# Optimization experiments

Hardware: AMD Instinct MI355X
Metric: run time of the kernel (lower is better)

Reference implementation:

```python
import jax, jax.numpy as jnp
import numpy as np

MARGIN = 0.2

def _pdist(a, b):
    # euclidean distance matrix, matches pdist_torch (clamp at 1e-12 then sqrt)
    d2 = (a * a).sum(1)[:, None] + (b * b).sum(1)[None, :] - 2.0 * (a @ b.T)
    return jnp.sqrt(jnp.clip(d2, 1e-12))

def setup_inputs() -> dict:
    key = jax.random.key(0)
    P, K, D = 128, 16, 4096  # identities, samples-per-identity, feature dim
    inputs = jax.random.normal(key, (4 * P * K, D), dtype=jnp.float32)
    # labels laid out [modality, identity, sample] so torch.chunk grouping is valid
    targets = jnp.tile(jnp.repeat(jnp.arange(P, dtype=jnp.int64), K), 4)
    return {"inputs": inputs, "targets": targets, "num_classes": P}

def reference(inputs, targets, num_classes):
    P = int(num_classes)
    total, D = inputs.shape
    K = total // (4 * P)
    # per-modality, per-identity centers: [4, P, D]
    c = inputs.reshape(4, P, K, D).mean(axis=2)
    c1, c2, c3, c4 = c[0], c[1], c[2], c[3]

    eye = jnp.eye(P, dtype=bool)
    offdiag_min = lambda d: jnp.min(jnp.where(eye, jnp.inf, d), axis=1)
    # unique labels => mask is identity => masked max/min over mask[i] is the diagonal
    ap123 = jnp.diagonal(_pdist(c2, c3))
    an123 = jax.lax.stop_gradient(jnp.diagonal(_pdist(c1, c3)))  # .detach()
    an33 = offdiag_min(_pdist(c3, c3))
    an11 = offdiag_min(_pdist(c1, c1))
    ap124 = jnp.diagonal(_pdist(c1, c4))
    an124 = jax.lax.stop_gradient(jnp.diagonal(_pdist(c2, c4)))  # .detach()
    an44 = offdiag_min(_pdist(c4, c4))
    an22 = offdiag_min(_pdist(c2, c2))

    # MarginRankingLoss(margin)(x1=an, x2=ap, y=1) = mean(relu(ap - an + margin))
    mrl = lambda an, ap: jnp.mean(jnp.maximum(ap - an + MARGIN, 0.0))
    loss_123 = mrl(an123, ap123) + 0.5 * (mrl(an33, ap123) + mrl(an11, ap123))
    loss_124 = mrl(an124, ap124) + 0.5 * (mrl(an44, ap124) + mrl(an22, ap124))
    return (loss_123 + loss_124) / 2
```

## Files before the change

kernel.cpp:

```cpp
#include <hip/hip_runtime.h>
#include <math.h>

#define P_IDS 128
#define D_DIM 4096
#define MARGIN_F 0.2f
#define NCHUNK 32

__global__ __launch_bounds__(128) void centers_kernel(const float* __restrict__ in,
                                                      float* __restrict__ c, int K) {
    const int b  = blockIdx.x;
    const int ds = blockIdx.y;
    const float* src = in + (size_t)b * K * D_DIM + ds * 512;
    float* dst = c + (size_t)b * D_DIM + ds * 512;
    const float inv = 1.0f / (float)K;
    float4 acc = make_float4(0.f, 0.f, 0.f, 0.f);
    const int t = threadIdx.x;
    for (int k = 0; k < K; ++k) {
        float4 v = reinterpret_cast<const float4*>(src + (size_t)k * D_DIM)[t];
        acc.x += v.x; acc.y += v.y; acc.z += v.z; acc.w += v.w;
    }
    acc.x *= inv; acc.y *= inv; acc.z *= inv; acc.w *= inv;
    reinterpret_cast<float4*>(dst)[t] = acc;
}

__global__ __launch_bounds__(256) void pair_partial_kernel(const float* __restrict__ c,
                                                           float* __restrict__ part) {
    __shared__ float As[64][68];
    __shared__ float Bs[64][68];
    const int tid = threadIdx.x;
    const int tx = tid & 15, ty = tid >> 4;
    const int bx = blockIdx.x;
    const int m = bx >> 2, it = (bx >> 1) & 1, jt = bx & 1;
    const int dc = blockIdx.y;
    const float* cm = c + (size_t)m * P_IDS * D_DIM;
    const float* gA = cm + (size_t)(it * 64) * D_DIM;
    const float* gB = cm + (size_t)(jt * 64) * D_DIM;

    float acc[4][4];
    #pragma unroll
    for (int r = 0; r < 4; ++r)
        #pragma unroll
        for (int s = 0; s < 4; ++s) acc[r][s] = 0.f;

    for (int ch = 0; ch < 2; ++ch) {
        const int dbase = dc * 128 + ch * 64;
        __syncthreads();
        #pragma unroll
        for (int idx = 0; idx < 4; ++idx) {
            int li = idx * 256 + tid;
            int row = li >> 4, c4 = li & 15;
            float4 va = *reinterpret_cast<const float4*>(gA + (size_t)row * D_DIM + dbase + c4 * 4);
            float4 vb = *reinterpret_cast<const float4*>(gB + (size_t)row * D_DIM + dbase + c4 * 4);
            *reinterpret_cast<float4*>(&As[row][c4 * 4]) = va;
            *reinterpret_cast<float4*>(&Bs[row][c4 * 4]) = vb;
        }
        __syncthreads();
        #pragma unroll
        for (int d4 = 0; d4 < 16; ++d4) {
            float4 a[4], b[4];
            #pragma unroll
            for (int r = 0; r < 4; ++r)
                a[r] = *reinterpret_cast<const float4*>(&As[ty * 4 + r][d4 * 4]);
            #pragma unroll
            for (int s = 0; s < 4; ++s)
                b[s] = *reinterpret_cast<const float4*>(&Bs[s * 16 + tx][d4 * 4]);
            #pragma unroll
            for (int r = 0; r < 4; ++r)
                #pragma unroll
                for (int s = 0; s < 4; ++s) {
                    float dx = a[r].x - b[s].x, dy = a[r].y - b[s].y;
                    float dz = a[r].z - b[s].z, dw = a[r].w - b[s].w;
                    acc[r][s] = fmaf(dx, dx, acc[r][s]);
                    acc[r][s] = fmaf(dy, dy, acc[r][s]);
                    acc[r][s] = fmaf(dz, dz, acc[r][s]);
                    acc[r][s] = fmaf(dw, dw, acc[r][s]);
                }
        }
    }
    float* pbase = part + ((size_t)dc * 4 + m) * P_IDS * P_IDS;
    #pragma unroll
    for (int r = 0; r < 4; ++r) {
        int i = it * 64 + ty * 4 + r;
        #pragma unroll
        for (int s = 0; s < 4; ++s) {
            int j = jt * 64 + s * 16 + tx;
            pbase[i * P_IDS + j] = acc[r][s];
        }
    }
}

__global__ __launch_bounds__(256) void rowmin_kernel(const float* __restrict__ part,
                                                     float* __restrict__ anmin) {
    const int tid = threadIdx.x;
    const int rowid = blockIdx.x * 2 + (tid >> 7);
    const int j = tid & 127;
    const size_t base = (size_t)rowid * P_IDS + j;
    float sum = 0.f;
    #pragma unroll 4
    for (int dc = 0; dc < NCHUNK; ++dc)
        sum += part[(size_t)dc * 4 * P_IDS * P_IDS + base];
    float d = sqrtf(fmaxf(sum, 1e-12f));
    if (j == (rowid & (P_IDS - 1))) d = INFINITY;
    #pragma unroll
    for (int off = 32; off > 0; off >>= 1) d = fminf(d, __shfl_down(d, off, 64));
    __shared__ float wmin[4];
    if ((tid & 63) == 0) wmin[tid >> 6] = d;
    __syncthreads();
    if (tid == 0) {
        anmin[blockIdx.x * 2]     = fminf(wmin[0], wmin[1]);
        anmin[blockIdx.x * 2 + 1] = fminf(wmin[2], wmin[3]);
    }
}

__global__ __launch_bounds__(256) void diag_kernel(const float* __restrict__ c,
                                                   float* __restrict__ diag) {
    const int i = blockIdx.x;
    const size_t PD = (size_t)P_IDS * D_DIM;
    const float4* r1 = reinterpret_cast<const float4*>(c + 0 * PD + (size_t)i * D_DIM);
    const float4* r2 = reinterpret_cast<const float4*>(c + 1 * PD + (size_t)i * D_DIM);
    const float4* r3 = reinterpret_cast<const float4*>(c + 2 * PD + (size_t)i * D_DIM);
    const float4* r4 = reinterpret_cast<const float4*>(c + 3 * PD + (size_t)i * D_DIM);
    float a23 = 0.f, a13 = 0.f, a14 = 0.f, a24 = 0.f;
    for (int t = threadIdx.x; t < (D_DIM >> 2); t += 256) {
        float4 v1 = r1[t], v2 = r2[t], v3 = r3[t], v4 = r4[t];
        float dx, dy, dz, dw;
        dx = v2.x - v3.x; dy = v2.y - v3.y; dz = v2.z - v3.z; dw = v2.w - v3.w;
        a23 = fmaf(dx, dx, a23); a23 = fmaf(dy, dy, a23);
        a23 = fmaf(dz, dz, a23); a23 = fmaf(dw, dw, a23);
        dx = v1.x - v3.x; dy = v1.y - v3.y; dz = v1.z - v3.z; dw = v1.w - v3.w;
        a13 = fmaf(dx, dx, a13); a13 = fmaf(dy, dy, a13);
        a13 = fmaf(dz, dz, a13); a13 = fmaf(dw, dw, a13);
        dx = v1.x - v4.x; dy = v1.y - v4.y; dz = v1.z - v4.z; dw = v1.w - v4.w;
        a14 = fmaf(dx, dx, a14); a14 = fmaf(dy, dy, a14);
        a14 = fmaf(dz, dz, a14); a14 = fmaf(dw, dw, a14);
        dx = v2.x - v4.x; dy = v2.y - v4.y; dz = v2.z - v4.z; dw = v2.w - v4.w;
        a24 = fmaf(dx, dx, a24); a24 = fmaf(dy, dy, a24);
        a24 = fmaf(dz, dz, a24); a24 = fmaf(dw, dw, a24);
    }
    const int wave = threadIdx.x >> 6, lane = threadIdx.x & 63;
    #pragma unroll
    for (int off = 32; off > 0; off >>= 1) {
        a23 += __shfl_down(a23, off, 64);
        a13 += __shfl_down(a13, off, 64);
        a14 += __shfl_down(a14, off, 64);
        a24 += __shfl_down(a24, off, 64);
    }
    __shared__ float red[4][4];
    if (lane == 0) { red[wave][0] = a23; red[wave][1] = a13; red[wave][2] = a14; red[wave][3] = a24; }
    __syncthreads();
    if (threadIdx.x == 0) {
        float s23 = red[0][0] + red[1][0] + red[2][0] + red[3][0];
        float s13 = red[0][1] + red[1][1] + red[2][1] + red[3][1];
        float s14 = red[0][2] + red[1][2] + red[2][2] + red[3][2];
        float s24 = red[0][3] + red[1][3] + red[2][3] + red[3][3];
        diag[0 * P_IDS + i] = sqrtf(fmaxf(s23, 1e-12f));
        diag[1 * P_IDS + i] = sqrtf(fmaxf(s13, 1e-12f));
        diag[2 * P_IDS + i] = sqrtf(fmaxf(s14, 1e-12f));
        diag[3 * P_IDS + i] = sqrtf(fmaxf(s24, 1e-12f));
    }
}

__global__ __launch_bounds__(128) void loss_kernel(const float* __restrict__ anmin,
                                                   const float* __restrict__ diag,
                                                   float* __restrict__ out) {
    const int i = threadIdx.x;
    float ap123 = diag[0 * P_IDS + i], an123 = diag[1 * P_IDS + i];
    float ap124 = diag[2 * P_IDS + i], an124 = diag[3 * P_IDS + i];
    float an11 = anmin[0 * P_IDS + i], an22 = anmin[1 * P_IDS + i];
    float an33 = anmin[2 * P_IDS + i], an44 = anmin[3 * P_IDS + i];
    float s = fmaxf(ap123 - an123 + MARGIN_F, 0.f)
            + 0.5f * (fmaxf(ap123 - an33 + MARGIN_F, 0.f) +
                      fmaxf(ap123 - an11 + MARGIN_F, 0.f))
            + fmaxf(ap124 - an124 + MARGIN_F, 0.f)
            + 0.5f * (fmaxf(ap124 - an44 + MARGIN_F, 0.f) +
                      fmaxf(ap124 - an22 + MARGIN_F, 0.f));
    #pragma unroll
    for (int off = 32; off > 0; off >>= 1) s += __shfl_down(s, off, 64);
    __shared__ float w[2];
    if ((threadIdx.x & 63) == 0) w[threadIdx.x >> 6] = s;
    __syncthreads();
    if (threadIdx.x == 0) out[0] = (w[0] + w[1]) / (2.0f * (float)P_IDS);
}

extern "C" void kernel_launch(void* const* d_in, const int* in_sizes, int n_in,
                              void* d_out, int out_size, void* d_ws, size_t ws_size,
                              hipStream_t stream) {
    const float* in = (const float*)d_in[0];
    const int N = in_sizes[1];
    const int K = N / (4 * P_IDS);

    float* c     = (float*)d_ws;
    float* part  = c + (size_t)4 * P_IDS * D_DIM;
    float* anmin = part + (size_t)NCHUNK * 4 * P_IDS * P_IDS;
    float* diag  = anmin + 4 * P_IDS;

    hipLaunchKernelGGL(centers_kernel, dim3(4 * P_IDS, 8), dim3(128), 0, stream, in, c, K);
    hipLaunchKernelGGL(pair_partial_kernel, dim3(16, NCHUNK), dim3(256), 0, stream, c, part);
    hipLaunchKernelGGL(rowmin_kernel, dim3(2 * P_IDS), dim3(256), 0, stream, part, anmin);
    hipLaunchKernelGGL(diag_kernel, dim3(P_IDS), dim3(256), 0, stream, c, diag);
    hipLaunchKernelGGL(loss_kernel, dim3(1), dim3(128), 0, stream, anmin, diag, (float*)d_out);
}
```

Measured before the change: 52.50 us.

## Fuse all stages into one cooperative persistent kernel with grid syncs

Replaces the five separate kernel launches with a single cooperative kernel of 256 blocks × 512 threads that runs centers, pairwise partial distances, row-min and diagonal reductions, and the final loss, separated by grid.sync(). The number of reduction chunks drops from 32 to 16 to fit the 256-block grid, which halves the partial-buffer traffic, and the diagonal distances are split one pair per wave. The aim is to remove per-launch overhead and inter-kernel gaps. In exchange it pays grid-wide barrier costs, uses fewer, larger blocks in the pair phase, and falls back to four ordinary launches if the cooperative launch fails.

```diff
diff --git a/kernel.cpp b/kernel.cpp
--- a/kernel.cpp
+++ b/kernel.cpp
@@ -1,71 +1,82 @@
 #include <hip/hip_runtime.h>
+#include <hip/hip_cooperative_groups.h>
 #include <math.h>
+
+namespace cg = cooperative_groups;
 
 #define P_IDS 128
 #define D_DIM 4096
+#define K_SMP 16
 #define MARGIN_F 0.2f
-#define NCHUNK 32
-
-__global__ __launch_bounds__(128) void centers_kernel(const float* __restrict__ in,
-                                                      float* __restrict__ c, int K) {
-    const int b  = blockIdx.x;
-    const int ds = blockIdx.y;
-    const float* src = in + (size_t)b * K * D_DIM + ds * 512;
-    float* dst = c + (size_t)b * D_DIM + ds * 512;
-    const float inv = 1.0f / (float)K;
-    float4 acc = make_float4(0.f, 0.f, 0.f, 0.f);
-    const int t = threadIdx.x;
-    for (int k = 0; k < K; ++k) {
-        float4 v = reinterpret_cast<const float4*>(src + (size_t)k * D_DIM)[t];
-        acc.x += v.x; acc.y += v.y; acc.z += v.z; acc.w += v.w;
-    }
-    acc.x *= inv; acc.y *= inv; acc.z *= inv; acc.w *= inv;
-    reinterpret_cast<float4*>(dst)[t] = acc;
-}
-
-__global__ __launch_bounds__(256) void pair_partial_kernel(const float* __restrict__ c,
-                                                           float* __restrict__ part) {
-    __shared__ float As[64][68];
-    __shared__ float Bs[64][68];
-    const int tid = threadIdx.x;
+#define NCHUNK 16
+
+__device__ __forceinline__ void dev_centers(const float* __restrict__ in,
+                                            float* __restrict__ c,
+                                            int blk, int tid) {
+    const float inv = 1.0f / (float)K_SMP;
+    #pragma unroll
+    for (int r = 0; r < 2; ++r) {
+        const int row = blk * 2 + r;
+        const float* src = in + (size_t)row * K_SMP * D_DIM;
+        float* dst = c + (size_t)row * D_DIM;
+        float4 acc0 = make_float4(0.f, 0.f, 0.f, 0.f);
+        float4 acc1 = make_float4(0.f, 0.f, 0.f, 0.f);
+        #pragma unroll 4
+        for (int k = 0; k < K_SMP; ++k) {
+            const float4* s4 = reinterpret_cast<const float4*>(src + (size_t)k * D_DIM);
+            float4 v0 = s4[tid], v1 = s4[512 + tid];
+            acc0.x += v0.x; acc0.y += v0.y; acc0.z += v0.z; acc0.w += v0.w;
+            acc1.x += v1.x; acc1.y += v1.y; acc1.z += v1.z; acc1.w += v1.w;
+        }
+        acc0.x *= inv; acc0.y *= inv; acc0.z *= inv; acc0.w *= inv;
+        acc1.x *= inv; acc1.y *= inv; acc1.z *= inv; acc1.w *= inv;
+        reinterpret_cast<float4*>(dst)[tid]       = acc0;
+        reinterpret_cast<float4*>(dst)[512 + tid] = acc1;
+    }
+}
+
+__device__ __forceinline__ void dev_pair(const float* __restrict__ c,
+                                         float* __restrict__ part,
+                                         int blk, int tid,
+                                         float (*As)[68], float (*Bs)[68]) {
+    const int bx = blk & 15;
+    const int dc = blk >> 4;
+    const int m = bx >> 2, it = (bx >> 1) & 1, jt = bx & 1;
     const int tx = tid & 15, ty = tid >> 4;
-    const int bx = blockIdx.x;
-    const int m = bx >> 2, it = (bx >> 1) & 1, jt = bx & 1;
-    const int dc = blockIdx.y;
     const float* cm = c + (size_t)m * P_IDS * D_DIM;
     const float* gA = cm + (size_t)(it * 64) * D_DIM;
     const float* gB = cm + (size_t)(jt * 64) * D_DIM;
 
-    float acc[4][4];
-    #pragma unroll
-    for (int r = 0; r < 4; ++r)
+    float acc[2][4];
+    #pragma unroll
+    for (int r = 0; r < 2; ++r)
         #pragma unroll
         for (int s = 0; s < 4; ++s) acc[r][s] = 0.f;
 
-    for (int ch = 0; ch < 2; ++ch) {
-        const int dbase = dc * 128 + ch * 64;
+    for (int ch = 0; ch < 4; ++ch) {
+        const int dbase = dc * 256 + ch * 64;
         __syncthreads();
         #pragma unroll
-        for (int idx = 0; idx < 4; ++idx) {
-            int li = idx * 256 + tid;
+        for (int idx = 0; idx < 2; ++idx) {
+            int li = idx * 512 + tid;
             int row = li >> 4, c4 = li & 15;
-            float4 va = *reinterpret_cast<const float4*>(gA + (size_t)row * D_DIM + dbase + c4 * 4);
-            float4 vb = *reinterpret_cast<const float4*>(gB + (size_t)row * D_DIM + dbase + c4 * 4);
-            *reinterpret_cast<float4*>(&As[row][c4 * 4]) = va;
-            *reinterpret_cast<float4*>(&Bs[row][c4 * 4]) = vb;
+            *reinterpret_cast<float4*>(&As[row][c4 * 4]) =
+                *reinterpret_cast<const float4*>(gA + (size_t)row * D_DIM + dbase + c4 * 4);
+            *reinterpret_cast<float4*>(&Bs[row][c4 * 4]) =
+                *reinterpret_cast<const float4*>(gB + (size_t)row * D_DIM + dbase + c4 * 4);
         }
         __syncthreads();
         #pragma unroll
         for (int d4 = 0; d4 < 16; ++d4) {
-            float4 a[4], b[4];
+            float4 a[2], b[4];
             #pragma unroll
-            for (int r = 0; r < 4; ++r)
-                a[r] = *reinterpret_cast<const float4*>(&As[ty * 4 + r][d4 * 4]);
+            for (int r = 0; r < 2; ++r)
+                a[r] = *reinterpret_cast<const float4*>(&As[ty * 2 + r][d4 * 4]);
             #pragma unroll
             for (int s = 0; s < 4; ++s)
                 b[s] = *reinterpret_cast<const float4*>(&Bs[s * 16 + tx][d4 * 4]);
             #pragma unroll
-            for (int r = 0; r < 4; ++r)
+            for (int r = 0; r < 2; ++r)
                 #pragma unroll
                 for (int s = 0; s < 4; ++s) {
                     float dx = a[r].x - b[s].x, dy = a[r].y - b[s].y;
@@ -77,10 +88,10 @@
                 }
         }
     }
-    float* pbase = part + ((size_t)dc * 4 + m) * P_IDS * P_IDS;
-    #pragma unroll
-    for (int r = 0; r < 4; ++r) {
-        int i = it * 64 + ty * 4 + r;
+    float* pbase = part + ((size_t)dc * 4 + m) * (P_IDS * P_IDS);
+    #pragma unroll
+    for (int r = 0; r < 2; ++r) {
+        int i = it * 64 + ty * 2 + r;
         #pragma unroll
         for (int s = 0; s < 4; ++s) {
             int j = jt * 64 + s * 16 + tx;
@@ -89,114 +100,150 @@
     }
 }
 
-__global__ __launch_bounds__(256) void rowmin_kernel(const float* __restrict__ part,
-                                                     float* __restrict__ anmin) {
-    const int tid = threadIdx.x;
-    const int rowid = blockIdx.x * 2 + (tid >> 7);
-    const int j = tid & 127;
-    const size_t base = (size_t)rowid * P_IDS + j;
-    float sum = 0.f;
-    #pragma unroll 4
-    for (int dc = 0; dc < NCHUNK; ++dc)
-        sum += part[(size_t)dc * 4 * P_IDS * P_IDS + base];
-    float d = sqrtf(fmaxf(sum, 1e-12f));
-    if (j == (rowid & (P_IDS - 1))) d = INFINITY;
+__device__ __forceinline__ void dev_rowmin(const float* __restrict__ part,
+                                           float* __restrict__ anmin,
+                                           int blk, int tid) {
+    __shared__ float wmin[8];
+    float d = INFINITY;
+    if (tid < 256) {
+        const int rowid = blk * 2 + (tid >> 7);
+        const int j = tid & 127;
+        const size_t base = (size_t)(rowid >> 7) * (P_IDS * P_IDS) +
+                            (size_t)(rowid & 127) * P_IDS + j;
+        float sum = 0.f;
+        #pragma unroll 4
+        for (int dc = 0; dc < NCHUNK; ++dc)
+            sum += part[(size_t)dc * 4 * P_IDS * P_IDS + base];
+        d = sqrtf(fmaxf(sum, 1e-12f));
+        if (j == (rowid & (P_IDS - 1))) d = INFINITY;
+    }
     #pragma unroll
     for (int off = 32; off > 0; off >>= 1) d = fminf(d, __shfl_down(d, off, 64));
-    __shared__ float wmin[4];
     if ((tid & 63) == 0) wmin[tid >> 6] = d;
     __syncthreads();
     if (tid == 0) {
-        anmin[blockIdx.x * 2]     = fminf(wmin[0], wmin[1]);
-        anmin[blockIdx.x * 2 + 1] = fminf(wmin[2], wmin[3]);
-    }
-}
-
-__global__ __launch_bounds__(256) void diag_kernel(const float* __restrict__ c,
-                                                   float* __restrict__ diag) {
-    const int i = blockIdx.x;
+        anmin[blk * 2]     = fminf(wmin[0], wmin[1]);
+        anmin[blk * 2 + 1] = fminf(wmin[2], wmin[3]);
+    }
+}
+
+__device__ __forceinline__ void dev_diag(const float* __restrict__ c,
+                                         float* __restrict__ diag,
+                                         int i, int tid) {
+    const int wave = tid >> 6, lane = tid & 63;
+    if (wave >= 4) return;
+    const int am = (wave == 0 || wave == 3) ? 1 : 0;
+    const int bm = (wave <= 1) ? 2 : 3;
     const size_t PD = (size_t)P_IDS * D_DIM;
-    const float4* r1 = reinterpret_cast<const float4*>(c + 0 * PD + (size_t)i * D_DIM);
-    const float4* r2 = reinterpret_cast<const float4*>(c + 1 * PD + (size_t)i * D_DIM);
-    const float4* r3 = reinterpret_cast<const float4*>(c + 2 * PD + (size_t)i * D_DIM);
-    const float4* r4 = reinterpret_cast<const float4*>(c + 3 * PD + (size_t)i * D_DIM);
-    float a23 = 0.f, a13 = 0.f, a14 = 0.f, a24 = 0.f;
-    for (int t = threadIdx.x; t < (D_DIM >> 2); t += 256) {
-        float4 v1 = r1[t], v2 = r2[t], v3 = r3[t], v4 = r4[t];
-        float dx, dy, dz, dw;
-        dx = v2.x - v3.x; dy = v2.y - v3.y; dz = v2.z - v3.z; dw = v2.w - v3.w;
-        a23 = fmaf(dx, dx, a23); a23 = fmaf(dy, dy, a23);
-        a23 = fmaf(dz, dz, a23); a23 = fmaf(dw, dw, a23);
-        dx = v1.x - v3.x; dy = v1.y - v3.y; dz = v1.z - v3.z; dw = v1.w - v3.w;
-        a13 = fmaf(dx, dx, a13); a13 = fmaf(dy, dy, a13);
-        a13 = fmaf(dz, dz, a13); a13 = fmaf(dw, dw, a13);
-        dx = v1.x - v4.x; dy = v1.y - v4.y; dz = v1.z - v4.z; dw = v1.w - v4.w;
-        a14 = fmaf(dx, dx, a14); a14 = fmaf(dy, dy, a14);
-        a14 = fmaf(dz, dz, a14); a14 = fmaf(dw, dw, a14);
-        dx = v2.x - v4.x; dy = v2.y - v4.y; dz = v2.z - v4.z; dw = v2.w - v4.w;
-        a24 = fmaf(dx, dx, a24); a24 = fmaf(dy, dy, a24);
-        a24 = fmaf(dz, dz, a24); a24 = fmaf(dw, dw, a24);
-    }
-    const int wave = threadIdx.x >> 6, lane = threadIdx.x & 63;
-    #pragma unroll
-    for (int off = 32; off > 0; off >>= 1) {
-        a23 += __shfl_down(a23, off, 64);
-        a13 += __shfl_down(a13, off, 64);
-        a14 += __shfl_down(a14, off, 64);
-        a24 += __shfl_down(a24, off, 64);
-    }
-    __shared__ float red[4][4];
-    if (lane == 0) { red[wave][0] = a23; red[wave][1] = a13; red[wave][2] = a14; red[wave][3] = a24; }
+    const float4* ra = reinterpret_cast<const float4*>(c + am * PD + (size_t)i * D_DIM);
+    const float4* rb = reinterpret_cast<const float4*>(c + bm * PD + (size_t)i * D_DIM);
+    float acc = 0.f;
+    #pragma unroll
+    for (int t = 0; t < 16; ++t) {
+        float4 a = ra[t * 64 + lane];
+        float4 b = rb[t * 64 + lane];
+        float dx = a.x - b.x, dy = a.y - b.y, dz = a.z - b.z, dw = a.w - b.w;
+        acc = fmaf(dx, dx, acc); acc = fmaf(dy, dy, acc);
+        acc = fmaf(dz, dz, acc); acc = fmaf(dw, dw, acc);
+    }
+    #pragma unroll
+    for (int off = 32; off > 0; off >>= 1) acc += __shfl_down(acc, off, 64);
+    if (lane == 0) diag[wave * P_IDS + i] = sqrtf(fmaxf(acc, 1e-12f));
+}
+
+__device__ __forceinline__ void dev_loss(const float* __restrict__ anmin,
+                                         const float* __restrict__ diag,
+                                         float* __restrict__ out, int tid) {
+    __shared__ float w[8];
+    float s = 0.f;
+    if (tid < 128) {
+        const int i = tid;
+        float ap123 = diag[0 * P_IDS + i], an123 = diag[1 * P_IDS + i];
+        float ap124 = diag[2 * P_IDS + i], an124 = diag[3 * P_IDS + i];
+        float an11 = anmin[0 * P_IDS + i], an22 = anmin[1 * P_IDS + i];
+        float an33 = anmin[2 * P_IDS + i], an44 = anmin[3 * P_IDS + i];
+        s = fmaxf(ap123 - an123 + MARGIN_F, 0.f)
+          + 0.5f * (fmaxf(ap123 - an33 + MARGIN_F, 0.f) +
+                    fmaxf(ap123 - an11 + MARGIN_F, 0.f))
+          + fmaxf(ap124 - an124 + MARGIN_F, 0.f)
+          + 0.5f * (fmaxf(ap124 - an44 + MARGIN_F, 0.f) +
+                    fmaxf(ap124 - an22 + MARGIN_F, 0.f));
+    }
+    #pragma unroll
+    for (int off = 32; off > 0; off >>= 1) s += __shfl_down(s, off, 64);
+    if ((tid & 63) == 0) w[tid >> 6] = s;
     __syncthreads();
-    if (threadIdx.x == 0) {
-        float s23 = red[0][0] + red[1][0] + red[2][0] + red[3][0];
-        float s13 = red[0][1] + red[1][1] + red[2][1] + red[3][1];
-        float s14 = red[0][2] + red[1][2] + red[2][2] + red[3][2];
-        float s24 = red[0][3] + red[1][3] + red[2][3] + red[3][3];
-        diag[0 * P_IDS + i] = sqrtf(fmaxf(s23, 1e-12f));
-        diag[1 * P_IDS + i] = sqrtf(fmaxf(s13, 1e-12f));
-        diag[2 * P_IDS + i] = sqrtf(fmaxf(s14, 1e-12f));
-        diag[3 * P_IDS + i] = sqrtf(fmaxf(s24, 1e-12f));
-    }
-}
-
-__global__ __launch_bounds__(128) void loss_kernel(const float* __restrict__ anmin,
-                                                   const float* __restrict__ diag,
-                                                   float* __restrict__ out) {
-    const int i = threadIdx.x;
-    float ap123 = diag[0 * P_IDS + i], an123 = diag[1 * P_IDS + i];
-    float ap124 = diag[2 * P_IDS + i], an124 = diag[3 * P_IDS + i];
-    float an11 = anmin[0 * P_IDS + i], an22 = anmin[1 * P_IDS + i];
-    float an33 = anmin[2 * P_IDS + i], an44 = anmin[3 * P_IDS + i];
-    float s = fmaxf(ap123 - an123 + MARGIN_F, 0.f)
-            + 0.5f * (fmaxf(ap123 - an33 + MARGIN_F, 0.f) +
-                      fmaxf(ap123 - an11 + MARGIN_F, 0.f))
-            + fmaxf(ap124 - an124 + MARGIN_F, 0.f)
-            + 0.5f * (fmaxf(ap124 - an44 + MARGIN_F, 0.f) +
-                      fmaxf(ap124 - an22 + MARGIN_F, 0.f));
-    #pragma unroll
-    for (int off = 32; off > 0; off >>= 1) s += __shfl_down(s, off, 64);
-    __shared__ float w[2];
-    if ((threadIdx.x & 63) == 0) w[threadIdx.x >> 6] = s;
-    __syncthreads();
-    if (threadIdx.x == 0) out[0] = (w[0] + w[1]) / (2.0f * (float)P_IDS);
+    if (tid == 0)
+        out[0] = (w[0] + w[1] + w[2] + w[3] + w[4] + w[5] + w[6] + w[7])
+               / (2.0f * (float)P_IDS);
+}
+
+__global__ __launch_bounds__(512) void cpm_fused(const float* __restrict__ in,
+                                                 float* __restrict__ c,
+                                                 float* __restrict__ part,
+                                                 float* __restrict__ anmin,
+                                                 float* __restrict__ diag,
+                                                 float* __restrict__ out) {
+    cg::grid_group grid = cg::this_grid();
+    __shared__ float As[64][68];
+    __shared__ float Bs[64][68];
+    const int tid = threadIdx.x;
+    const int blk = blockIdx.x;
+
+    dev_centers(in, c, blk, tid);
+    grid.sync();
+    dev_pair(c, part, blk, tid, As, Bs);
+    grid.sync();
+    dev_rowmin(part, anmin, blk, tid);
+    if (blk < 128) dev_diag(c, diag, blk, tid);
+    grid.sync();
+    if (blk == 0) dev_loss(anmin, diag, out, tid);
+}
+
+__global__ __launch_bounds__(512) void k_centers(const float* __restrict__ in,
+                                                 float* __restrict__ c) {
+    dev_centers(in, c, blockIdx.x, threadIdx.x);
+}
+__global__ __launch_bounds__(512) void k_pair(const float* __restrict__ c,
+                                              float* __restrict__ part) {
+    __shared__ float As[64][68];
+    __shared__ float Bs[64][68];
+    dev_pair(c, part, blockIdx.x, threadIdx.x, As, Bs);
+}
+__global__ __launch_bounds__(512) void k_red(const float* __restrict__ part,
+                                             const float* __restrict__ c,
+                                             float* __restrict__ anmin,
+                                             float* __restrict__ diag) {
+    dev_rowmin(part, anmin, blockIdx.x, threadIdx.x);
+    if (blockIdx.x < 128) dev_diag(c, diag, blockIdx.x, threadIdx.x);
+}
+__global__ __launch_bounds__(512) void k_loss(const float* __restrict__ anmin,
+                                              const float* __restrict__ diag,
+                                              float* __restrict__ out) {
+    dev_loss(anmin, diag, out, threadIdx.x);
 }
 
 extern "C" void kernel_launch(void* const* d_in, const int* in_sizes, int n_in,
                               void* d_out, int out_size, void* d_ws, size_t ws_size,
                               hipStream_t stream) {
     const float* in = (const float*)d_in[0];
-    const int N = in_sizes[1];
-    const int K = N / (4 * P_IDS);
 
     float* c     = (float*)d_ws;
     float* part  = c + (size_t)4 * P_IDS * D_DIM;
     float* anmin = part + (size_t)NCHUNK * 4 * P_IDS * P_IDS;
     float* diag  = anmin + 4 * P_IDS;
-
-    hipLaunchKernelGGL(centers_kernel, dim3(4 * P_IDS, 8), dim3(128), 0, stream, in, c, K);
-    hipLaunchKernelGGL(pair_partial_kernel, dim3(16, NCHUNK), dim3(256), 0, stream, c, part);
-    hipLaunchKernelGGL(rowmin_kernel, dim3(2 * P_IDS), dim3(256), 0, stream, part, anmin);
-    hipLaunchKernelGGL(diag_kernel, dim3(P_IDS), dim3(256), 0, stream, c, diag);
-    hipLaunchKernelGGL(loss_kernel, dim3(1), dim3(128), 0, stream, anmin, diag, (float*)d_out);
-}
+    float* outp  = (float*)d_out;
+
+    void* args[] = {(void*)&in, (void*)&c, (void*)&part,
+                    (void*)&anmin, (void*)&diag, (void*)&outp};
+    hipError_t err = hipLaunchCooperativeKernel((const void*)cpm_fused,
+                                                dim3(256), dim3(512),
+                                                args, 0, stream);
+    if (err != hipSuccess) {
+        (void)hipGetLastError();
+        hipLaunchKernelGGL(k_centers, dim3(256), dim3(512), 0, stream, in, c);
+        hipLaunchKernelGGL(k_pair,    dim3(256), dim3(512), 0, stream, c, part);
+        hipLaunchKernelGGL(k_red,     dim3(256), dim3(512), 0, stream, part, c, anmin, diag);
+        hipLaunchKernelGGL(k_loss,    dim3(1),   dim3(512), 0, stream, anmin, diag, outp);
+    }
+}
```

Result: slower. 151.1 us (+187.9%).

## Fuse diagonal distances into centers kernel and merge rowmin with loss tail

Applied to the files above, without the earlier changes.

The centers kernel now processes all four modalities for one identity and one 256-column slab in each block. It computes the four cross-modality diagonal squared-distance partials from shared memory, so a separate diag kernel no longer has to re-read the centers. The rowmin and loss kernels are merged into one tail kernel that uses an atomic counter to pick a last block, which then reduces the diag partials and computes the loss. The sqrt is moved after the min reduction. Together these cut the launch count from five to three and remove one pass over the centers, at the cost of an atomic/threadfence handoff and a counter reset done inside the first kernel.

```diff
diff --git a/kernel.cpp b/kernel.cpp
--- a/kernel.cpp
+++ b/kernel.cpp
@@ -3,28 +3,60 @@
 
 #define P_IDS 128
 #define D_DIM 4096
+#define K_SMP 16
 #define MARGIN_F 0.2f
 #define NCHUNK 32
-
-__global__ __launch_bounds__(128) void centers_kernel(const float* __restrict__ in,
-                                                      float* __restrict__ c, int K) {
-    const int b  = blockIdx.x;
+#define NSLAB 16
+
+__global__ __launch_bounds__(256, 4) void k_centers(const float* __restrict__ in,
+                                                    float* __restrict__ c,
+                                                    float* __restrict__ dpart,
+                                                    int* __restrict__ cnt) {
+    __shared__ float Lc[4 * 256];
+    __shared__ float wred[4][4];
+    const int tid = threadIdx.x;
+    const int p  = blockIdx.x;
     const int ds = blockIdx.y;
-    const float* src = in + (size_t)b * K * D_DIM + ds * 512;
-    float* dst = c + (size_t)b * D_DIM + ds * 512;
-    const float inv = 1.0f / (float)K;
+    if (p == 0 && ds == 0 && tid == 0) *cnt = 0;
+    const int m = tid >> 6, lane = tid & 63;
+    const size_t colbase = (size_t)ds * 256 + lane * 4;
+
+    const float* src = in + (size_t)(m * P_IDS + p) * K_SMP * D_DIM + colbase;
     float4 acc = make_float4(0.f, 0.f, 0.f, 0.f);
-    const int t = threadIdx.x;
-    for (int k = 0; k < K; ++k) {
-        float4 v = reinterpret_cast<const float4*>(src + (size_t)k * D_DIM)[t];
+    #pragma unroll 4
+    for (int k = 0; k < K_SMP; ++k) {
+        float4 v = *reinterpret_cast<const float4*>(src + (size_t)k * D_DIM);
         acc.x += v.x; acc.y += v.y; acc.z += v.z; acc.w += v.w;
     }
+    const float inv = 1.0f / (float)K_SMP;
     acc.x *= inv; acc.y *= inv; acc.z *= inv; acc.w *= inv;
-    reinterpret_cast<float4*>(dst)[t] = acc;
-}
-
-__global__ __launch_bounds__(256) void pair_partial_kernel(const float* __restrict__ c,
-                                                           float* __restrict__ part) {
+    *reinterpret_cast<float4*>(c + (size_t)(m * P_IDS + p) * D_DIM + colbase) = acc;
+    *reinterpret_cast<float4*>(&Lc[m * 256 + lane * 4]) = acc;
+    __syncthreads();
+
+    float v0 = Lc[0 * 256 + tid], v1 = Lc[1 * 256 + tid];
+    float v2 = Lc[2 * 256 + tid], v3 = Lc[3 * 256 + tid];
+    float d0 = (v1 - v2) * (v1 - v2);
+    float d1 = (v0 - v2) * (v0 - v2);
+    float d2 = (v0 - v3) * (v0 - v3);
+    float d3 = (v1 - v3) * (v1 - v3);
+    #pragma unroll
+    for (int off = 32; off > 0; off >>= 1) {
+        d0 += __shfl_down(d0, off, 64);
+        d1 += __shfl_down(d1, off, 64);
+        d2 += __shfl_down(d2, off, 64);
+        d3 += __shfl_down(d3, off, 64);
+    }
+    if (lane == 0) { wred[m][0] = d0; wred[m][1] = d1; wred[m][2] = d2; wred[m][3] = d3; }
+    __syncthreads();
+    if (tid < 4) {
+        float s = wred[0][tid] + wred[1][tid] + wred[2][tid] + wred[3][tid];
+        dpart[((size_t)ds * 4 + tid) * P_IDS + p] = s;
+    }
+}
+
+__global__ __launch_bounds__(256) void k_pair(const float* __restrict__ c,
+                                              float* __restrict__ part) {
     __shared__ float As[64][68];
     __shared__ float Bs[64][68];
     const int tid = threadIdx.x;
@@ -49,10 +81,10 @@
         for (int idx = 0; idx < 4; ++idx) {
             int li = idx * 256 + tid;
             int row = li >> 4, c4 = li & 15;
-            float4 va = *reinterpret_cast<const float4*>(gA + (size_t)row * D_DIM + dbase + c4 * 4);
-            float4 vb = *reinterpret_cast<const float4*>(gB + (size_t)row * D_DIM + dbase + c4 * 4);
-            *reinterpret_cast<float4*>(&As[row][c4 * 4]) = va;
-            *reinterpret_cast<float4*>(&Bs[row][c4 * 4]) = vb;
+            *reinterpret_cast<float4*>(&As[row][c4 * 4]) =
+                *reinterpret_cast<const float4*>(gA + (size_t)row * D_DIM + dbase + c4 * 4);
+            *reinterpret_cast<float4*>(&Bs[row][c4 * 4]) =
+                *reinterpret_cast<const float4*>(gB + (size_t)row * D_DIM + dbase + c4 * 4);
         }
         __syncthreads();
         #pragma unroll
@@ -77,7 +109,7 @@
                 }
         }
     }
-    float* pbase = part + ((size_t)dc * 4 + m) * P_IDS * P_IDS;
+    float* pbase = part + ((size_t)dc * 4 + m) * (P_IDS * P_IDS);
     #pragma unroll
     for (int r = 0; r < 4; ++r) {
         int i = it * 64 + ty * 4 + r;
@@ -89,114 +121,88 @@
     }
 }
 
-__global__ __launch_bounds__(256) void rowmin_kernel(const float* __restrict__ part,
-                                                     float* __restrict__ anmin) {
+__global__ __launch_bounds__(256) void k_tail(const float* __restrict__ part,
+                                              const float* __restrict__ dpart,
+                                              float* __restrict__ anmin,
+                                              int* __restrict__ cnt,
+                                              float* __restrict__ out) {
+    __shared__ float wmin[4];
+    __shared__ float diagf[4 * P_IDS];
+    __shared__ float red[4];
+    __shared__ int lastflag;
     const int tid = threadIdx.x;
-    const int rowid = blockIdx.x * 2 + (tid >> 7);
+    const int blk = blockIdx.x;
+
+    const int rowid = blk * 2 + (tid >> 7);
     const int j = tid & 127;
     const size_t base = (size_t)rowid * P_IDS + j;
     float sum = 0.f;
     #pragma unroll 4
     for (int dc = 0; dc < NCHUNK; ++dc)
         sum += part[(size_t)dc * 4 * P_IDS * P_IDS + base];
-    float d = sqrtf(fmaxf(sum, 1e-12f));
-    if (j == (rowid & (P_IDS - 1))) d = INFINITY;
-    #pragma unroll
-    for (int off = 32; off > 0; off >>= 1) d = fminf(d, __shfl_down(d, off, 64));
-    __shared__ float wmin[4];
-    if ((tid & 63) == 0) wmin[tid >> 6] = d;
+    float d2 = fmaxf(sum, 1e-12f);
+    if (j == (rowid & (P_IDS - 1))) d2 = INFINITY;
+    #pragma unroll
+    for (int off = 32; off > 0; off >>= 1) d2 = fminf(d2, __shfl_down(d2, off, 64));
+    if ((tid & 63) == 0) wmin[tid >> 6] = d2;
     __syncthreads();
     if (tid == 0) {
-        anmin[blockIdx.x * 2]     = fminf(wmin[0], wmin[1]);
-        anmin[blockIdx.x * 2 + 1] = fminf(wmin[2], wmin[3]);
-    }
-}
-
-__global__ __launch_bounds__(256) void diag_kernel(const float* __restrict__ c,
-                                                   float* __restrict__ diag) {
-    const int i = blockIdx.x;
-    const size_t PD = (size_t)P_IDS * D_DIM;
-    const float4* r1 = reinterpret_cast<const float4*>(c + 0 * PD + (size_t)i * D_DIM);
-    const float4* r2 = reinterpret_cast<const float4*>(c + 1 * PD + (size_t)i * D_DIM);
-    const float4* r3 = reinterpret_cast<const float4*>(c + 2 * PD + (size_t)i * D_DIM);
-    const float4* r4 = reinterpret_cast<const float4*>(c + 3 * PD + (size_t)i * D_DIM);
-    float a23 = 0.f, a13 = 0.f, a14 = 0.f, a24 = 0.f;
-    for (int t = threadIdx.x; t < (D_DIM >> 2); t += 256) {
-        float4 v1 = r1[t], v2 = r2[t], v3 = r3[t], v4 = r4[t];
-        float dx, dy, dz, dw;
-        dx = v2.x - v3.x; dy = v2.y - v3.y; dz = v2.z - v3.z; dw = v2.w - v3.w;
-        a23 = fmaf(dx, dx, a23); a23 = fmaf(dy, dy, a23);
-        a23 = fmaf(dz, dz, a23); a23 = fmaf(dw, dw, a23);
-        dx = v1.x - v3.x; dy = v1.y - v3.y; dz = v1.z - v3.z; dw = v1.w - v3.w;
-        a13 = fmaf(dx, dx, a13); a13 = fmaf(dy, dy, a13);
-        a13 = fmaf(dz, dz, a13); a13 = fmaf(dw, dw, a13);
-        dx = v1.x - v4.x; dy = v1.y - v4.y; dz = v1.z - v4.z; dw = v1.w - v4.w;
-        a14 = fmaf(dx, dx, a14); a14 = fmaf(dy, dy, a14);
-        a14 = fmaf(dz, dz, a14); a14 = fmaf(dw, dw, a14);
-        dx = v2.x - v4.x; dy = v2.y - v4.y; dz = v2.z - v4.z; dw = v2.w - v4.w;
-        a24 = fmaf(dx, dx, a24); a24 = fmaf(dy, dy, a24);
-        a24 = fmaf(dz, dz, a24); a24 = fmaf(dw, dw, a24);
-    }
-    const int wave = threadIdx.x >> 6, lane = threadIdx.x & 63;
-    #pragma unroll
-    for (int off = 32; off > 0; off >>= 1) {
-        a23 += __shfl_down(a23, off, 64);
-        a13 += __shfl_down(a13, off, 64);
-        a14 += __shfl_down(a14, off, 64);
-        a24 += __shfl_down(a24, off, 64);
-    }
-    __shared__ float red[4][4];
-    if (lane == 0) { red[wave][0] = a23; red[wave][1] = a13; red[wave][2] = a14; red[wave][3] = a24; }
-    __syncthreads();
-    if (threadIdx.x == 0) {
-        float s23 = red[0][0] + red[1][0] + red[2][0] + red[3][0];
-        float s13 = red[0][1] + red[1][1] + red[2][1] + red[3][1];
-        float s14 = red[0][2] + red[1][2] + red[2][2] + red[3][2];
-        float s24 = red[0][3] + red[1][3] + red[2][3] + red[3][3];
-        diag[0 * P_IDS + i] = sqrtf(fmaxf(s23, 1e-12f));
-        diag[1 * P_IDS + i] = sqrtf(fmaxf(s13, 1e-12f));
-        diag[2 * P_IDS + i] = sqrtf(fmaxf(s14, 1e-12f));
-        diag[3 * P_IDS + i] = sqrtf(fmaxf(s24, 1e-12f));
-    }
-}
-
-__global__ __launch_bounds__(128) void loss_kernel(const float* __restrict__ anmin,
-                                                   const float* __restrict__ diag,
-                                                   float* __restrict__ out) {
-    const int i = threadIdx.x;
-    float ap123 = diag[0 * P_IDS + i], an123 = diag[1 * P_IDS + i];
-    float ap124 = diag[2 * P_IDS + i], an124 = diag[3 * P_IDS + i];
-    float an11 = anmin[0 * P_IDS + i], an22 = anmin[1 * P_IDS + i];
-    float an33 = anmin[2 * P_IDS + i], an44 = anmin[3 * P_IDS + i];
-    float s = fmaxf(ap123 - an123 + MARGIN_F, 0.f)
-            + 0.5f * (fmaxf(ap123 - an33 + MARGIN_F, 0.f) +
-                      fmaxf(ap123 - an11 + MARGIN_F, 0.f))
-            + fmaxf(ap124 - an124 + MARGIN_F, 0.f)
-            + 0.5f * (fmaxf(ap124 - an44 + MARGIN_F, 0.f) +
-                      fmaxf(ap124 - an22 + MARGIN_F, 0.f));
-    #pragma unroll
-    for (int off = 32; off > 0; off >>= 1) s += __shfl_down(s, off, 64);
-    __shared__ float w[2];
-    if ((threadIdx.x & 63) == 0) w[threadIdx.x >> 6] = s;
-    __syncthreads();
-    if (threadIdx.x == 0) out[0] = (w[0] + w[1]) / (2.0f * (float)P_IDS);
+        anmin[blk * 2]     = sqrtf(fminf(wmin[0], wmin[1]));
+        anmin[blk * 2 + 1] = sqrtf(fminf(wmin[2], wmin[3]));
+        __threadfence();
+        lastflag = (atomicAdd(cnt, 1) == 255);
+    }
+    __syncthreads();
+
+    if (lastflag) {
+        __threadfence();
+        #pragma unroll
+        for (int e = tid; e < 4 * P_IDS; e += 256) {
+            float s = 0.f;
+            #pragma unroll
+            for (int ds = 0; ds < NSLAB; ++ds)
+                s += dpart[(size_t)ds * 4 * P_IDS + e];
+            diagf[e] = sqrtf(fmaxf(s, 1e-12f));
+        }
+        __syncthreads();
+        float s = 0.f;
+        if (tid < 128) {
+            const int i = tid;
+            float ap123 = diagf[0 * P_IDS + i], an123 = diagf[1 * P_IDS + i];
+            float ap124 = diagf[2 * P_IDS + i], an124 = diagf[3 * P_IDS + i];
+            float an11 = anmin[0 * P_IDS + i], an22 = anmin[1 * P_IDS + i];
+            float an33 = anmin[2 * P_IDS + i], an44 = anmin[3 * P_IDS + i];
+            s = fmaxf(ap123 - an123 + MARGIN_F, 0.f)
+              + 0.5f * (fmaxf(ap123 - an33 + MARGIN_F, 0.f) +
+                        fmaxf(ap123 - an11 + MARGIN_F, 0.f))
+              + fmaxf(ap124 - an124 + MARGIN_F, 0.f)
+              + 0.5f * (fmaxf(ap124 - an44 + MARGIN_F, 0.f) +
+                        fmaxf(ap124 - an22 + MARGIN_F, 0.f));
+        }
+        #pragma unroll
+        for (int off = 32; off > 0; off >>= 1) s += __shfl_down(s, off, 64);
+        if ((tid & 63) == 0) red[tid >> 6] = s;
+        __syncthreads();
+        if (tid == 0)
+            out[0] = (red[0] + red[1] + red[2] + red[3]) / (2.0f * (float)P_IDS);
+    }
 }
 
 extern "C" void kernel_launch(void* const* d_in, const int* in_sizes, int n_in,
                               void* d_out, int out_size, void* d_ws, size_t ws_size,
                               hipStream_t stream) {
     const float* in = (const float*)d_in[0];
-    const int N = in_sizes[1];
-    const int K = N / (4 * P_IDS);
 
     float* c     = (float*)d_ws;
     float* part  = c + (size_t)4 * P_IDS * D_DIM;
-    float* anmin = part + (size_t)NCHUNK * 4 * P_IDS * P_IDS;
-    float* diag  = anmin + 4 * P_IDS;
-
-    hipLaunchKernelGGL(centers_kernel, dim3(4 * P_IDS, 8), dim3(128), 0, stream, in, c, K);
-    hipLaunchKernelGGL(pair_partial_kernel, dim3(16, NCHUNK), dim3(256), 0, stream, c, part);
-    hipLaunchKernelGGL(rowmin_kernel, dim3(2 * P_IDS), dim3(256), 0, stream, part, anmin);
-    hipLaunchKernelGGL(diag_kernel, dim3(P_IDS), dim3(256), 0, stream, c, diag);
-    hipLaunchKernelGGL(loss_kernel, dim3(1), dim3(128), 0, stream, anmin, diag, (float*)d_out);
-}
+    float* dpart = part + (size_t)NCHUNK * 4 * P_IDS * P_IDS;
+    float* anmin = dpart + (size_t)NSLAB * 4 * P_IDS;
+    int*   cnt   = (int*)(anmin + 4 * P_IDS);
+    float* outp  = (float*)d_out;
+
+    hipLaunchKernelGGL(k_centers, dim3(P_IDS, NSLAB), dim3(256), 0, stream,
+                       in, c, dpart, cnt);
+    hipLaunchKernelGGL(k_pair, dim3(16, NCHUNK), dim3(256), 0, stream, c, part);
+    hipLaunchKernelGGL(k_tail, dim3(256), dim3(256), 0, stream,
+                       part, dpart, anmin, cnt, outp);
+}
```

Result: slower. 60.65 us (+15.5%).
